# Optimization experiments

Hardware: AMD Instinct MI355X
Metric: run time of the kernel (lower is better)

The kernel has to match this reference:

```python
import jax, jax.numpy as jnp
import numpy as np

D = 2048
H = 16
HD = D // H  # 128
EPS = 1e-6
SCALE = HD ** -0.5


def rms_norm(x, w):
    var = jnp.mean(jnp.square(x), axis=-1, keepdims=True)
    return x * jax.lax.rsqrt(var + EPS) * w


def setup_inputs() -> dict:
    key = jax.random.key(0)
    ks = jax.random.split(key, 16)
    std = D ** -0.5
    B, P, S = 2, 1024, 2048
    inp = {
        "vision_features": jax.random.normal(ks[0], (B, P, D), jnp.float32),
        "language_features": jax.random.normal(ks[1], (B, S, D), jnp.float32),
        "vision_pos_embed": jax.random.normal(ks[2], (1, 1024, D), jnp.float32) * 0.02,
        "text_pos_embed": jax.random.normal(ks[3], (1, 2048, D), jnp.float32) * 0.02,
        "vision_norm_w": jnp.ones((D,), jnp.float32),
        "language_norm_w": jnp.ones((D,), jnp.float32),
    }
    wnames = ["w_vq", "w_vk", "w_vv", "w_lq", "w_lk", "w_lv", "w_v2l", "w_l2v", "w_out"]
    for i, n in enumerate(wnames):
        inp[n] = jax.random.normal(ks[4 + i], (D, D), jnp.float32) * std  # [out, in]
    return inp


def reference(vision_features, language_features, vision_pos_embed, text_pos_embed,
              vision_norm_w, language_norm_w,
              w_vq, w_vk, w_vv, w_lq, w_lk, w_lv, w_v2l, w_l2v, w_out):
    B, P, _ = vision_features.shape
    S = language_features.shape[1]

    vf = vision_features + vision_pos_embed[:, :P, :]
    lf = language_features + text_pos_embed[:, :S, :]

    vn = rms_norm(vf, vision_norm_w)
    ln = rms_norm(lf, language_norm_w)

    def proj(x, w):  # x [B,T,D], w [D,D] (out,in) -> [B,H,T,HD]
        y = jnp.einsum('btd,ed->bte', x, w)
        return y.reshape(x.shape[0], x.shape[1], H, HD).transpose(0, 2, 1, 3)

    v_q = proj(vn, w_vq) * SCALE
    v_k = proj(vn, w_vk)
    v_v = proj(vn, w_vv)
    l_q = proj(ln, w_lq) * SCALE
    l_k = proj(ln, w_lk)
    l_v = proj(ln, w_lv)

    # vision -> language cross attention: [B,H,P,S]
    v2l_scores = jnp.einsum('bhpd,bhsd->bhps', v_q, l_k)
    v2l_attn = jax.nn.softmax(v2l_scores.astype(jnp.float32), axis=-1).astype(vf.dtype)
    v2l_out = jnp.einsum('bhps,bhsd->bhpd', v2l_attn, l_v)
    v2l_out = v2l_out.transpose(0, 2, 1, 3).reshape(B, P, D)
    v2l_out = jnp.einsum('bpd,ed->bpe', v2l_out, w_v2l)

    # language -> vision cross attention: [B,H,S,P]
    l2v_scores = jnp.einsum('bhsd,bhpd->bhsp', l_q, v_k)
    l2v_attn = jax.nn.softmax(l2v_scores.astype(jnp.float32), axis=-1).astype(lf.dtype)
    l2v_out = jnp.einsum('bhsp,bhpd->bhsd', l2v_attn, v_v)
    l2v_out = l2v_out.transpose(0, 2, 1, 3).reshape(B, S, D)
    l2v_out = jnp.einsum('bsd,ed->bse', l2v_out, w_l2v)

    vision_output = vf + v2l_out
    language_output = lf + l2v_out
    fused = jnp.concatenate([vision_output, language_output], axis=1)
    fused_output = jnp.einsum('btd,ed->bte', fused, w_out)

    return fused_output, vision_output, language_output, v2l_attn
```

## Files before the change

### kernel.cpp

```cpp
#include <hip/hip_runtime.h>
#include <hip/hip_bf16.h>


typedef __bf16 b8 __attribute__((ext_vector_type(8)));
typedef float f4 __attribute__((ext_vector_type(4)));
typedef float f16v __attribute__((ext_vector_type(16)));
typedef unsigned int uint32;

#define MFMA_16(a,b,c) __builtin_amdgcn_mfma_f32_16x16x32_bf16(a,b,c,0,0,0)
#define MFMA_32(a,b,c) __builtin_amdgcn_mfma_f32_32x32x16_bf16(a,b,c,0,0,0)

__device__ __forceinline__ ushort f2bf(float f){
  uint32 u = __float_as_uint(f);
  return (ushort)((u + 0x7FFFu + ((u >> 16) & 1u)) >> 16);
}

__device__ __forceinline__ void async16(const void* g, void* l){
  __builtin_amdgcn_global_load_lds(
      (__attribute__((address_space(1))) void*)(g),
      (__attribute__((address_space(3))) void*)(l), 16, 0, 0);
}

__device__ __forceinline__ uint32 cvtpk(float a, float b){
  uint32 r;
  asm("v_cvt_pk_bf16_f32 %0, %1, %2" : "=v"(r) : "v"(a), "v"(b));
  return r;
}

struct CastArgs { const float* s[6]; ushort* d[6]; float sc[6]; int nseg; };

__global__ __launch_bounds__(256)
void cast_k(CastArgs a){
  int n = a.nseg << 20;
  for (int i = blockIdx.x*blockDim.x + threadIdx.x; i < n; i += gridDim.x*blockDim.x){
    int seg = i >> 20, off = i & 1048575;
    float4 v = reinterpret_cast<const float4*>(a.s[seg])[off];
    float sc = a.sc[seg];
    ushort4 o;
    o.x = f2bf(v.x*sc); o.y = f2bf(v.y*sc); o.z = f2bf(v.z*sc); o.w = f2bf(v.w*sc);
    reinterpret_cast<ushort4*>(a.d[seg])[off] = o;
  }
}

__global__ __launch_bounds__(256)
void prep_k(const float* __restrict__ vfeat, const float* __restrict__ lfeat,
            const float* __restrict__ vpos, const float* __restrict__ lpos,
            const float* __restrict__ vw, const float* __restrict__ lw,
            float* __restrict__ vfo, float* __restrict__ lfo,
            ushort* __restrict__ vnb, ushort* __restrict__ lnb)
{
  const int row = blockIdx.x;
  const float *src, *pos, *w;
  float* fo; ushort* nb;
  if (row < 2048){
    src = vfeat + (size_t)row*2048; pos = vpos + (size_t)(row & 1023)*2048;
    w = vw; fo = vfo + (size_t)row*2048; nb = vnb + (size_t)row*2048;
  } else {
    int r = row - 2048;
    src = lfeat + (size_t)r*2048; pos = lpos + (size_t)(r & 2047)*2048;
    w = lw; fo = lfo + (size_t)r*2048; nb = lnb + (size_t)r*2048;
  }
  const int t = threadIdx.x;
  float4 a0 = reinterpret_cast<const float4*>(src)[t];
  float4 p0 = reinterpret_cast<const float4*>(pos)[t];
  float4 a1 = reinterpret_cast<const float4*>(src)[t+256];
  float4 p1 = reinterpret_cast<const float4*>(pos)[t+256];
  a0.x += p0.x; a0.y += p0.y; a0.z += p0.z; a0.w += p0.w;
  a1.x += p1.x; a1.y += p1.y; a1.z += p1.z; a1.w += p1.w;
  float ss = a0.x*a0.x + a0.y*a0.y + a0.z*a0.z + a0.w*a0.w
           + a1.x*a1.x + a1.y*a1.y + a1.z*a1.z + a1.w*a1.w;
  #pragma unroll
  for (int o = 32; o > 0; o >>= 1) ss += __shfl_xor(ss, o, 64);
  __shared__ float red[4];
  if ((t & 63) == 0) red[t >> 6] = ss;
  __syncthreads();
  float rs = rsqrtf((red[0]+red[1]+red[2]+red[3]) * (1.0f/2048.0f) + 1e-6f);
  reinterpret_cast<float4*>(fo)[t]     = a0;
  reinterpret_cast<float4*>(fo)[t+256] = a1;
  float4 w0 = reinterpret_cast<const float4*>(w)[t];
  float4 w1 = reinterpret_cast<const float4*>(w)[t+256];
  ushort4 o0, o1;
  o0.x = f2bf(a0.x*rs*w0.x); o0.y = f2bf(a0.y*rs*w0.y);
  o0.z = f2bf(a0.z*rs*w0.z); o0.w = f2bf(a0.w*rs*w0.w);
  o1.x = f2bf(a1.x*rs*w1.x); o1.y = f2bf(a1.y*rs*w1.y);
  o1.z = f2bf(a1.z*rs*w1.z); o1.w = f2bf(a1.w*rs*w1.w);
  reinterpret_cast<ushort4*>(nb)[t]     = o0;
  reinterpret_cast<ushort4*>(nb)[t+256] = o1;
}

template<int MODE>
__global__ __launch_bounds__(256, 3)
void gemm_k(const ushort* __restrict__ A, const ushort* __restrict__ A2,
            const ushort* __restrict__ W, ushort* __restrict__ OB,
            ushort* __restrict__ VT, float* __restrict__ OF, int logT)
{
  __shared__ __align__(16) ushort As[4096];
  __shared__ __align__(16) ushort Bs[4096];
  const int tid = threadIdx.x;
  const int l = tid & 63, wid = tid >> 6;
  const int wm = (wid >> 1) * 64, wn = (wid & 1) * 64;
  const int m0 = blockIdx.y * 128, n0 = blockIdx.x * 128;
  const int lr = l & 15, lk = l >> 4;
  f4 acc[4][4] = {};
  for (int kt = 0; kt < 2048; kt += 32) {
    #pragma unroll
    for (int i = 0; i < 2; ++i){
      int c = wid*64 + l + i*256;
      int row = c >> 2, kc = (c & 3) * 8;
      const ushort* ga;
      if constexpr (MODE == 2) {
        int f = m0 + row;
        int bb = (f >= 3072) ? 1 : 0;
        int rr = f - bb*3072;
        ga = (rr < 1024) ? (A  + ((size_t)(bb*1024 + rr))*2048 + kt + kc)
                         : (A2 + ((size_t)(bb*2048 + rr - 1024))*2048 + kt + kc);
      } else {
        ga = A + (size_t)(m0 + row)*2048 + kt + kc;
      }
      async16(ga, &As[c*8]);
      async16(W + (size_t)(n0 + row)*2048 + kt + kc, &Bs[c*8]);
    }
    __syncthreads();
    b8 af[4], bfr[4];
    #pragma unroll
    for (int i = 0; i < 4; ++i)
      af[i] = *reinterpret_cast<const b8*>(&As[(wm + i*16 + lr)*32 + lk*8]);
    #pragma unroll
    for (int j = 0; j < 4; ++j)
      bfr[j] = *reinterpret_cast<const b8*>(&Bs[(wn + j*16 + lr)*32 + lk*8]);
    #pragma unroll
    for (int i = 0; i < 4; ++i)
      #pragma unroll
      for (int j = 0; j < 4; ++j)
        acc[i][j] = MFMA_16(af[i], bfr[j], acc[i][j]);
    __syncthreads();
  }
  #pragma unroll
  for (int i = 0; i < 4; ++i){
    int row0 = m0 + wm + i*16 + lk*4;
    #pragma unroll
    for (int j = 0; j < 4; ++j){
      int col = n0 + wn + j*16 + lr;
      if constexpr (MODE == 0){
        if (col < 4096){
          #pragma unroll
          for (int r = 0; r < 4; ++r)
            OB[(size_t)(row0 + r)*4096 + col] = f2bf(acc[i][j][r]);
        } else {
          int d = col - 4096, hh = d >> 7, dd = d & 127;
          int bb = row0 >> logT;
          int t0 = row0 - (bb << logT);
          ushort4 pk;
          pk.x = f2bf(acc[i][j][0]); pk.y = f2bf(acc[i][j][1]);
          pk.z = f2bf(acc[i][j][2]); pk.w = f2bf(acc[i][j][3]);
          *reinterpret_cast<ushort4*>(
              &VT[(((size_t)(bb*16 + hh)*128 + dd) << logT) + t0]) = pk;
        }
      } else if constexpr (MODE == 1){
        #pragma unroll
        for (int r = 0; r < 4; ++r){
          size_t idx = (size_t)(row0 + r)*2048 + col;
          float v = acc[i][j][r] + OF[idx];
          OF[idx] = v;
          OB[idx] = f2bf(v);
        }
      } else {
        #pragma unroll
        for (int r = 0; r < 4; ++r)
          OF[(size_t)(row0 + r)*2048 + col] = acc[i][j][r];
      }
    }
  }
}

template<int SKV, int WARPS, bool WA>
__global__ __launch_bounds__(WARPS*64, 2)
void attn_k(const ushort* __restrict__ qbuf, const ushort* __restrict__ kbuf,
            const ushort* __restrict__ vtb, float* __restrict__ attn,
            ushort* __restrict__ ctx, int TQ)
{
  constexpr int NT = SKV / 32;
  constexpr int NI = 512 / (WARPS*64);
  __shared__ __align__(16) ushort Ks[2][4096];
  __shared__ __align__(16) ushort Vs[2][4096];
  __shared__ __align__(16) float ast[WA ? WARPS*32*36 : 4];
  __shared__ float linv[WARPS*32];
  const int tid = threadIdx.x;
  const int l = tid & 63, wid = tid >> 6;
  const int hi = l >> 5, q = l & 31;
  const int b = blockIdx.z, h = blockIdx.y;
  const int q0 = blockIdx.x*(WARPS*32) + wid*32;
  const ushort* kbase = kbuf + (size_t)b*SKV*4096 + 2048 + h*128;
  const ushort* vbase = vtb + ((size_t)(b*16 + h))*128*SKV;

  b8 qf[8];
  {
    const ushort* qp = qbuf + (size_t)(b*TQ + q0 + q)*4096 + h*128 + hi*8;
    #pragma unroll
    for (int kd = 0; kd < 8; ++kd)
      qf[kd] = *reinterpret_cast<const b8*>(qp + kd*16);
  }

  #define STK(tt, bi) { int S0_ = (tt)*32; _Pragma("unroll") \
    for (int i_ = 0; i_ < NI; ++i_){ \
      int c_ = wid*64 + l + i_*(WARPS*64); int s_ = c_>>4, g_ = c_&15; \
      async16(kbase + (size_t)(S0_+s_)*4096 + (g_^(s_&15))*8, &Ks[bi][c_*8]); } }
  #define STV(tt, bi) { int S0_ = (tt)*32; _Pragma("unroll") \
    for (int i_ = 0; i_ < NI; ++i_){ \
      int c_ = wid*64 + l + i_*(WARPS*64); int d_ = c_>>2, g_ = c_&3; \
      async16(vbase + (size_t)d_*SKV + S0_ + (g_^(d_&3))*8, &Vs[bi][c_*8]); } }

  float mrun = -1e30f, lrun = 0.0f;
  STK(0, 0);
  for (int t = 0; t < NT; ++t){
    __syncthreads();
    if (t+1 < NT) STK(t+1, (t+1)&1);
    f16v s16 = {};
    #pragma unroll
    for (int kd = 0; kd < 8; ++kd){
      int gg = (kd*2 + hi) ^ (q & 15);
      b8 kf = *reinterpret_cast<const b8*>(&Ks[t&1][q*128 + gg*8]);
      s16 = MFMA_32(kf, qf[kd], s16);
    }
    float tm = s16[0];
    #pragma unroll
    for (int r = 1; r < 16; ++r) tm = fmaxf(tm, s16[r]);
    float mnew = fmaxf(mrun, tm);
    float sum = 0.f;
    #pragma unroll
    for (int r = 0; r < 16; ++r) sum += exp2f(s16[r] - mnew);
    lrun = lrun * exp2f(mrun - mnew) + sum;
    mrun = mnew;
  }
  {
    float mo = __shfl_xor(mrun, 32, 64);
    float lo = __shfl_xor(lrun, 32, 64);
    float mf = fmaxf(mrun, mo);
    lrun = lrun * exp2f(mrun - mf) + lo * exp2f(mo - mf);
    mrun = mf;
  }
  float invl = 1.0f / lrun;
  if (hi == 0) linv[wid*32 + q] = invl;
  __syncthreads();
  STK(0, 0); STV(0, 0);

  f16v O[4] = {};
  for (int t = 0; t < NT; ++t){
    __syncthreads();
    if (t+1 < NT){ STK(t+1, (t+1)&1); STV(t+1, (t+1)&1); }
    const int bi = t & 1;
    f16v s16 = {};
    #pragma unroll
    for (int kd = 0; kd < 8; ++kd){
      int gg = (kd*2 + hi) ^ (q & 15);
      b8 kf = *reinterpret_cast<const b8*>(&Ks[bi][q*128 + gg*8]);
      s16 = MFMA_32(kf, qf[kd], s16);
    }
    float e[16];
    #pragma unroll
    for (int r = 0; r < 16; ++r) e[r] = exp2f(s16[r] - mrun);
    if constexpr (WA){
      float* myt = &ast[wid*32*36];
      #pragma unroll
      for (int r = 0; r < 16; ++r){
        int sr = (r&3) + 8*(r>>2) + 4*hi;
        myt[q*36 + sr] = e[r] * invl;
      }
    }
    #pragma unroll
    for (int ks = 0; ks < 2; ++ks){
      const int base = ks*8;
      uint32 A0 = cvtpk(e[base+0], e[base+1]);
      uint32 A1 = cvtpk(e[base+2], e[base+3]);
      uint32 B0 = cvtpk(e[base+4], e[base+5]);
      uint32 B1 = cvtpk(e[base+6], e[base+7]);
      uint32 A0x = (uint32)__shfl_xor((int)A0, 32, 64);
      uint32 A1x = (uint32)__shfl_xor((int)A1, 32, 64);
      uint32 B0x = (uint32)__shfl_xor((int)B0, 32, 64);
      uint32 B1x = (uint32)__shfl_xor((int)B1, 32, 64);
      uint4 ww;
      ww.x = hi ? B0x : A0;
      ww.y = hi ? B1x : A1;
      ww.z = hi ? B0  : A0x;
      ww.w = hi ? B1  : A1x;
      b8 pa = __builtin_bit_cast(b8, ww);
      #pragma unroll
      for (int nb = 0; nb < 4; ++nb){
        int d = nb*32 + q;
        int gg2 = (ks*2 + hi) ^ (d & 3);
        b8 vfr = *reinterpret_cast<const b8*>(&Vs[bi][d*32 + gg2*8]);
        O[nb] = MFMA_32(pa, vfr, O[nb]);
      }
    }
    if constexpr (WA){
      const float* myt = &ast[wid*32*36];
      size_t abase = ((size_t)(b*16 + h)*TQ + q0) * SKV + t*32;
      #pragma unroll
      for (int it = 0; it < 4; ++it){
        int qq = (l >> 3) + it*8;
        float4 vv = *reinterpret_cast<const float4*>(&myt[qq*36 + (l&7)*4]);
        *reinterpret_cast<float4*>(&attn[abase + (size_t)qq*SKV + (l&7)*4]) = vv;
      }
    }
  }
  #pragma unroll
  for (int nb = 0; nb < 4; ++nb){
    #pragma unroll
    for (int r = 0; r < 16; ++r){
      int lq = (r&3) + 8*(r>>2) + 4*hi;
      float val = O[nb][r] * linv[wid*32 + lq];
      ctx[(size_t)(b*TQ + q0 + lq)*2048 + h*128 + nb*32 + q] = f2bf(val);
    }
  }
  #undef STK
  #undef STV
}

extern "C" void kernel_launch(void* const* d_in, const int* in_sizes, int n_in,
                              void* d_out, int out_size, void* d_ws, size_t ws_size,
                              hipStream_t stream)
{
  (void)in_sizes; (void)n_in; (void)out_size; (void)ws_size;
  const float* vfeat = (const float*)d_in[0];
  const float* lfeat = (const float*)d_in[1];
  const float* vpos  = (const float*)d_in[2];
  const float* lpos  = (const float*)d_in[3];
  const float* vw    = (const float*)d_in[4];
  const float* lw    = (const float*)d_in[5];
  const float* w_vq  = (const float*)d_in[6];
  const float* w_vk  = (const float*)d_in[7];
  const float* w_vv  = (const float*)d_in[8];
  const float* w_lq  = (const float*)d_in[9];
  const float* w_lk  = (const float*)d_in[10];
  const float* w_lv  = (const float*)d_in[11];
  const float* w_v2l = (const float*)d_in[12];
  const float* w_l2v = (const float*)d_in[13];
  const float* w_out = (const float*)d_in[14];

  float* out     = (float*)d_out;
  float* fused_o = out;
  float* vis_o   = out + 12582912;
  float* lan_o   = out + 16777216;
  float* attn_o  = out + 25165824;

  ushort* ws = (ushort*)d_ws;
  ushort* wcat_v = ws;
  ushort* wcat_l = wcat_v + 12582912;
  ushort* vnb    = wcat_l + 12582912;
  ushort* lnb    = vnb + 4194304;
  ushort* vqk    = lnb + 8388608;
  ushort* lqk    = vqk + 8388608;
  ushort* vtv    = lqk + 16777216;
  ushort* vtl    = vtv + 4194304;
  ushort* vctx    = wcat_v;
  ushort* lctx    = wcat_v + 4194304;
  ushort* w_v2l_b = wcat_l;
  ushort* w_l2v_b = wcat_l + 4194304;
  ushort* w_out_b = wcat_l + 8388608;

  const float QS = 0.08838834764831845f * 1.4426950408889634f;

  {
    CastArgs a;
    a.s[0]=w_vq; a.d[0]=wcat_v;           a.sc[0]=QS;
    a.s[1]=w_vk; a.d[1]=wcat_v+4194304;   a.sc[1]=1.f;
    a.s[2]=w_vv; a.d[2]=wcat_v+8388608;   a.sc[2]=1.f;
    a.s[3]=w_lq; a.d[3]=wcat_l;           a.sc[3]=QS;
    a.s[4]=w_lk; a.d[4]=wcat_l+4194304;   a.sc[4]=1.f;
    a.s[5]=w_lv; a.d[5]=wcat_l+8388608;   a.sc[5]=1.f;
    a.nseg = 6;
    cast_k<<<2048,256,0,stream>>>(a);
  }
  prep_k<<<6144,256,0,stream>>>(vfeat,lfeat,vpos,lpos,vw,lw,vis_o,lan_o,vnb,lnb);
  gemm_k<0><<<dim3(48,16),256,0,stream>>>(vnb,nullptr,wcat_v,vqk,vtv,nullptr,10);
  gemm_k<0><<<dim3(48,32),256,0,stream>>>(lnb,nullptr,wcat_l,lqk,vtl,nullptr,11);
  {
    CastArgs a;
    a.s[0]=w_v2l; a.d[0]=w_v2l_b; a.sc[0]=1.f;
    a.s[1]=w_l2v; a.d[1]=w_l2v_b; a.sc[1]=1.f;
    a.s[2]=w_out; a.d[2]=w_out_b; a.sc[2]=1.f;
    a.nseg = 3;
    cast_k<<<2048,256,0,stream>>>(a);
  }
  attn_k<2048,4,true ><<<dim3( 8,16,2),256,0,stream>>>(vqk,lqk,vtl,attn_o,vctx,1024);
  attn_k<1024,4,false><<<dim3(16,16,2),256,0,stream>>>(lqk,vqk,vtv,nullptr,lctx,2048);
  gemm_k<1><<<dim3(16,16),256,0,stream>>>(vctx,nullptr,w_v2l_b,vnb,nullptr,vis_o,0);
  gemm_k<1><<<dim3(16,32),256,0,stream>>>(lctx,nullptr,w_l2v_b,lnb,nullptr,lan_o,0);
  gemm_k<2><<<dim3(16,48),256,0,stream>>>(vnb,lnb,w_out_b,nullptr,nullptr,fused_o,0);
}
```

Measured before the change: 1.189 ms.

## Add 256x256 double-buffered 8-wave GEMM for QKV and output projections

Introduces a new GEMM kernel with 256x256 tiles, 512 threads, 64-wide K steps, double-buffered LDS with XOR swizzle, interleaved async loads and MFMA phases with priority hints, and a grouped block-index remap for cache locality. It replaces the 128x128 GEMM for the QKV projections and the final output projection, while the old kernel keeps only the residual-add mode. The aim is higher data reuse and overlap of global loads with MFMA compute, at the cost of a large LDS footprint (128KB), heavy register use, and fewer workgroups.

New measurement: 1.181 ms. Within noise of the previous version (-0.7%).

```diff
diff --git a/kernel.cpp b/kernel.cpp
--- a/kernel.cpp
+++ b/kernel.cpp
@@ -107,16 +107,7 @@
     for (int i = 0; i < 2; ++i){
       int c = wid*64 + l + i*256;
       int row = c >> 2, kc = (c & 3) * 8;
-      const ushort* ga;
-      if constexpr (MODE == 2) {
-        int f = m0 + row;
-        int bb = (f >= 3072) ? 1 : 0;
-        int rr = f - bb*3072;
-        ga = (rr < 1024) ? (A  + ((size_t)(bb*1024 + rr))*2048 + kt + kc)
-                         : (A2 + ((size_t)(bb*2048 + rr - 1024))*2048 + kt + kc);
-      } else {
-        ga = A + (size_t)(m0 + row)*2048 + kt + kc;
-      }
+      const ushort* ga = A + (size_t)(m0 + row)*2048 + kt + kc;
       async16(ga, &As[c*8]);
       async16(W + (size_t)(n0 + row)*2048 + kt + kc, &Bs[c*8]);
     }
@@ -141,36 +132,188 @@
     #pragma unroll
     for (int j = 0; j < 4; ++j){
       int col = n0 + wn + j*16 + lr;
+      #pragma unroll
+      for (int r = 0; r < 4; ++r){
+        size_t idx = (size_t)(row0 + r)*2048 + col;
+        float v = acc[i][j][r] + OF[idx];
+        OF[idx] = v;
+        OB[idx] = f2bf(v);
+      }
+    }
+  }
+}
+
+template<int MODE>
+__global__ __launch_bounds__(512, 2)
+void gemm8_k(const ushort* __restrict__ A, const ushort* __restrict__ A2,
+             const ushort* __restrict__ W, ushort* __restrict__ OB,
+             ushort* __restrict__ VT, float* __restrict__ OF, int logT)
+{
+  __shared__ __align__(16) ushort Ls[65536];
+  const int tid = threadIdx.x;
+  const int l = tid & 63, wid = tid >> 6;
+  const int wmid = wid >> 2, wnid = wid & 3;
+  const int lrow = l & 15, lg = l >> 4, lx = l & 7;
+
+  const int nbx = gridDim.x;
+  const int nwg = nbx * gridDim.y;
+  const int wg  = blockIdx.y*nbx + blockIdx.x;
+  const int swz = (wg & 7)*(nwg >> 3) + (wg >> 3);
+  const int m0 = (swz / nbx) * 256, n0 = (swz % nbx) * 256;
+
+  const ushort* srcA[2][2];
+  const ushort* srcB[2][2];
+  int ldsOff[2];
+  #pragma unroll
+  for (int i = 0; i < 2; ++i){
+    int c = tid + i*512;
+    int r = c >> 3, gs = c & 7;
+    int scol = (gs ^ (r & 7)) * 8;
+    ldsOff[i] = c * 8;
+    #pragma unroll
+    for (int hh = 0; hh < 2; ++hh){
+      int growA = m0 + hh*128 + r;
+      const ushort* pa;
+      if constexpr (MODE == 2){
+        int bb = (growA >= 3072) ? 1 : 0;
+        int rr = growA - bb*3072;
+        pa = (rr < 1024) ? (A  + (size_t)(bb*1024 + rr)*2048)
+                         : (A2 + (size_t)(bb*2048 + rr - 1024)*2048);
+      } else {
+        pa = A + (size_t)growA*2048;
+      }
+      srcA[hh][i] = pa + scol;
+      srcB[hh][i] = W + (size_t)(n0 + hh*128 + r)*2048 + scol;
+    }
+  }
+
+  #define STA8(hh, tt) { int bo_ = ((tt)&1)*32768; _Pragma("unroll") \
+    for (int i_ = 0; i_ < 2; ++i_) \
+      async16(srcA[hh][i_] + (tt)*64, &Ls[bo_ + (hh)*8192 + ldsOff[i_]]); }
+  #define STB8(hh, tt) { int bo_ = ((tt)&1)*32768; _Pragma("unroll") \
+    for (int i_ = 0; i_ < 2; ++i_) \
+      async16(srcB[hh][i_] + (tt)*64, &Ls[bo_ + 16384 + (hh)*8192 + ldsOff[i_]]); }
+
+  const int aBase = wmid*8192 + lrow*64;
+  const int bBase = 16384 + (wnid>>1)*8192 + (wnid&1)*4096 + lrow*64;
+  int gsw[2];
+  gsw[0] = ((0*4 + lg) ^ lx) * 8;
+  gsw[1] = ((1*4 + lg) ^ lx) * 8;
+
+  constexpr int NT = 32;
+  STB8(0,0); STB8(1,0); STA8(0,0); STA8(1,0); STB8(0,1); STB8(1,1); STA8(0,1);
+  asm volatile("s_waitcnt vmcnt(6)" ::: "memory");
+  __builtin_amdgcn_s_barrier();
+
+  f4 acc[8][4] = {};
+  b8 afr[4][2], b0r[2][2], b1r[2][2];
+
+  for (int t = 0; t < NT; ++t){
+    const ushort* Lb = &Ls[(t & 1) * 32768];
+    #pragma unroll
+    for (int mi = 0; mi < 4; ++mi)
+      #pragma unroll
+      for (int kk = 0; kk < 2; ++kk)
+        afr[mi][kk] = *reinterpret_cast<const b8*>(&Lb[aBase + mi*1024 + gsw[kk]]);
+    #pragma unroll
+    for (int nj = 0; nj < 2; ++nj)
+      #pragma unroll
+      for (int kk = 0; kk < 2; ++kk)
+        b0r[nj][kk] = *reinterpret_cast<const b8*>(&Lb[bBase + nj*1024 + gsw[kk]]);
+    if (t+1 < NT) STA8(1, t+1);
+    __builtin_amdgcn_s_barrier();
+    asm volatile("s_waitcnt lgkmcnt(0)" ::: "memory");
+    __builtin_amdgcn_s_setprio(1);
+    #pragma unroll
+    for (int mi = 0; mi < 4; ++mi)
+      #pragma unroll
+      for (int nj = 0; nj < 2; ++nj)
+        #pragma unroll
+        for (int kk = 0; kk < 2; ++kk)
+          acc[mi][nj] = MFMA_16(afr[mi][kk], b0r[nj][kk], acc[mi][nj]);
+    __builtin_amdgcn_s_setprio(0);
+    __builtin_amdgcn_s_barrier();
+    #pragma unroll
+    for (int nj = 0; nj < 2; ++nj)
+      #pragma unroll
+      for (int kk = 0; kk < 2; ++kk)
+        b1r[nj][kk] = *reinterpret_cast<const b8*>(&Lb[bBase + (2+nj)*1024 + gsw[kk]]);
+    __builtin_amdgcn_s_barrier();
+    asm volatile("s_waitcnt lgkmcnt(0)" ::: "memory");
+    __builtin_amdgcn_s_setprio(1);
+    #pragma unroll
+    for (int mi = 0; mi < 4; ++mi)
+      #pragma unroll
+      for (int nj = 0; nj < 2; ++nj)
+        #pragma unroll
+        for (int kk = 0; kk < 2; ++kk)
+          acc[mi][2+nj] = MFMA_16(afr[mi][kk], b1r[nj][kk], acc[mi][2+nj]);
+    __builtin_amdgcn_s_setprio(0);
+    __builtin_amdgcn_s_barrier();
+    #pragma unroll
+    for (int mi = 0; mi < 4; ++mi)
+      #pragma unroll
+      for (int kk = 0; kk < 2; ++kk)
+        afr[mi][kk] = *reinterpret_cast<const b8*>(&Lb[aBase + 4096 + mi*1024 + gsw[kk]]);
+    if (t+2 < NT) STB8(0, t+2);
+    __builtin_amdgcn_s_barrier();
+    asm volatile("s_waitcnt lgkmcnt(0)" ::: "memory");
+    __builtin_amdgcn_s_setprio(1);
+    #pragma unroll
+    for (int mi = 0; mi < 4; ++mi)
+      #pragma unroll
+      for (int nj = 0; nj < 2; ++nj)
+        #pragma unroll
+        for (int kk = 0; kk < 2; ++kk)
+          acc[4+mi][nj] = MFMA_16(afr[mi][kk], b0r[nj][kk], acc[4+mi][nj]);
+    __builtin_amdgcn_s_setprio(0);
+    __builtin_amdgcn_s_barrier();
+    if (t+2 < NT){ STB8(1, t+2); STA8(0, t+2); }
+    __builtin_amdgcn_s_barrier();
+    __builtin_amdgcn_s_setprio(1);
+    #pragma unroll
+    for (int mi = 0; mi < 4; ++mi)
+      #pragma unroll
+      for (int nj = 0; nj < 2; ++nj)
+        #pragma unroll
+        for (int kk = 0; kk < 2; ++kk)
+          acc[4+mi][2+nj] = MFMA_16(afr[mi][kk], b1r[nj][kk], acc[4+mi][2+nj]);
+    __builtin_amdgcn_s_setprio(0);
+    if (t+2 < NT){ asm volatile("s_waitcnt vmcnt(6)" ::: "memory"); }
+    else         { asm volatile("s_waitcnt vmcnt(0)" ::: "memory"); }
+    __builtin_amdgcn_s_barrier();
+  }
+
+  #pragma unroll
+  for (int mi = 0; mi < 8; ++mi){
+    int row0 = m0 + wmid*128 + mi*16 + lg*4;
+    #pragma unroll
+    for (int nj = 0; nj < 4; ++nj){
+      int col = n0 + wnid*64 + nj*16 + lrow;
       if constexpr (MODE == 0){
         if (col < 4096){
           #pragma unroll
           for (int r = 0; r < 4; ++r)
-            OB[(size_t)(row0 + r)*4096 + col] = f2bf(acc[i][j][r]);
+            OB[(size_t)(row0 + r)*4096 + col] = f2bf(acc[mi][nj][r]);
         } else {
           int d = col - 4096, hh = d >> 7, dd = d & 127;
           int bb = row0 >> logT;
           int t0 = row0 - (bb << logT);
           ushort4 pk;
-          pk.x = f2bf(acc[i][j][0]); pk.y = f2bf(acc[i][j][1]);
-          pk.z = f2bf(acc[i][j][2]); pk.w = f2bf(acc[i][j][3]);
+          pk.x = f2bf(acc[mi][nj][0]); pk.y = f2bf(acc[mi][nj][1]);
+          pk.z = f2bf(acc[mi][nj][2]); pk.w = f2bf(acc[mi][nj][3]);
           *reinterpret_cast<ushort4*>(
               &VT[(((size_t)(bb*16 + hh)*128 + dd) << logT) + t0]) = pk;
-        }
-      } else if constexpr (MODE == 1){
-        #pragma unroll
-        for (int r = 0; r < 4; ++r){
-          size_t idx = (size_t)(row0 + r)*2048 + col;
-          float v = acc[i][j][r] + OF[idx];
-          OF[idx] = v;
-          OB[idx] = f2bf(v);
         }
       } else {
         #pragma unroll
         for (int r = 0; r < 4; ++r)
-          OF[(size_t)(row0 + r)*2048 + col] = acc[i][j][r];
+          OF[(size_t)(row0 + r)*2048 + col] = acc[mi][nj][r];
       }
     }
   }
+  #undef STA8
+  #undef STB8
 }
 
 template<int SKV, int WARPS, bool WA>
@@ -372,8 +515,8 @@
     cast_k<<<2048,256,0,stream>>>(a);
   }
   prep_k<<<6144,256,0,stream>>>(vfeat,lfeat,vpos,lpos,vw,lw,vis_o,lan_o,vnb,lnb);
-  gemm_k<0><<<dim3(48,16),256,0,stream>>>(vnb,nullptr,wcat_v,vqk,vtv,nullptr,10);
-  gemm_k<0><<<dim3(48,32),256,0,stream>>>(lnb,nullptr,wcat_l,lqk,vtl,nullptr,11);
+  gemm8_k<0><<<dim3(24,8 ),512,0,stream>>>(vnb,nullptr,wcat_v,vqk,vtv,nullptr,10);
+  gemm8_k<0><<<dim3(24,16),512,0,stream>>>(lnb,nullptr,wcat_l,lqk,vtl,nullptr,11);
   {
     CastArgs a;
     a.s[0]=w_v2l; a.d[0]=w_v2l_b; a.sc[0]=1.f;
@@ -386,5 +529,5 @@
   attn_k<1024,4,false><<<dim3(16,16,2),256,0,stream>>>(lqk,vqk,vtv,nullptr,lctx,2048);
   gemm_k<1><<<dim3(16,16),256,0,stream>>>(vctx,nullptr,w_v2l_b,vnb,nullptr,vis_o,0);
   gemm_k<1><<<dim3(16,32),256,0,stream>>>(lctx,nullptr,w_l2v_b,lnb,nullptr,lan_o,0);
-  gemm_k<2><<<dim3(16,48),256,0,stream>>>(vnb,lnb,w_out_b,nullptr,nullptr,fused_o,0);
-}
+  gemm8_k<2><<<dim3(8,24),512,0,stream>>>(vnb,lnb,w_out_b,nullptr,nullptr,fused_o,0);
+}
```
